# Kernel optimization log

Measured on AMD Instinct MI355X. Metric: run time of the kernel, lower is better.

The kernel has to match this reference:

```python
import jax, jax.numpy as jnp
import numpy as np

B, N, D, H = 2, 2048, 384, 8
Dh = D // H          # 48
G = Dh // 3          # 16 3-vectors per head
EPS = 1e-5


def setup_inputs() -> dict:
    key = jax.random.key(0)
    ks = jax.random.split(key, 8)
    x = jax.random.normal(ks[0], (B, N, D), dtype=jnp.float32)
    # per-node SE(3) frames: proper rotation matrices via QR of random Gaussians
    raw = jax.random.normal(ks[1], (B, N, 3, 3), dtype=jnp.float32)
    q, r = jnp.linalg.qr(raw)
    sign = jnp.sign(jnp.diagonal(r, axis1=-2, axis2=-1))
    frames = q * sign[..., None, :]
    s = 1.0 / np.sqrt(D)
    Wq = jax.random.normal(ks[2], (D, D), dtype=jnp.float32) * s
    Wk = jax.random.normal(ks[3], (D, D), dtype=jnp.float32) * s
    Wv = jax.random.normal(ks[4], (D, D), dtype=jnp.float32) * s
    Wo = jax.random.normal(ks[5], (D, D), dtype=jnp.float32) * s
    bo = jnp.zeros((D,), dtype=jnp.float32)
    gamma = jnp.ones((D,), dtype=jnp.float32)
    beta = jnp.zeros((D,), dtype=jnp.float32)
    return {"x": x, "frames": frames, "Wq": Wq, "Wk": Wk, "Wv": Wv,
            "Wo": Wo, "bo": bo, "gamma": gamma, "beta": beta}


def _rotate(frames, t):
    # t: [B,N,H,Dh] -> rotate each 3-vector chunk by the node's frame R_i
    b, n, h, dh = t.shape
    t3 = t.reshape(b, n, h, dh // 3, 3)
    r3 = jnp.einsum('bnij,bnhgj->bnhgi', frames, t3)
    return r3.reshape(b, n, h, dh)


def reference(x, frames, Wq, Wk, Wv, Wo, bo, gamma, beta):
    b, n, d = x.shape
    Q = (x @ Wq.T).reshape(b, n, H, Dh)
    K = (x @ Wk.T).reshape(b, n, H, Dh)
    V = (x @ Wv.T).reshape(b, n, H, Dh)
    # SE(3) frame-conditioned attention: rotate Q,K into each node's local frame
    Qr = _rotate(frames, Q)
    Kr = _rotate(frames, K)
    scores = jnp.einsum('bqhd,bkhd->bhqk', Qr, Kr) / np.sqrt(Dh)
    attn = jax.nn.softmax(scores, axis=-1)
    out = jnp.einsum('bhqk,bkhd->bqhd', attn, V).reshape(b, n, d)
    out = out @ Wo.T + bo          # out_proj; dropout is identity in eval
    y = x + out                     # residual
    mu = jnp.mean(y, axis=-1, keepdims=True)
    var = jnp.var(y, axis=-1, keepdims=True)
    return (y - mu) * jax.lax.rsqrt(var + EPS) * gamma + beta
```

## Files before the change

kernel.cpp:

```cpp
#include <hip/hip_runtime.h>
#include <hip/hip_bf16.h>
#include <math.h>

constexpr int B = 2, N = 2048, D = 384, H = 8, Dh = 48;
constexpr int M = B * N;
constexpr float EPS = 1e-5f;
constexpr int WSZ = 384 * 384;

typedef short bf16x8 __attribute__((ext_vector_type(8)));
typedef float f32x4 __attribute__((ext_vector_type(4)));

#if __has_builtin(__builtin_amdgcn_exp2f)
#define EXP2(x) __builtin_amdgcn_exp2f(x)
#else
#define EXP2(x) exp2f(x)
#endif

__device__ __forceinline__ ushort f2bf(float f) {
  union { float f; uint u; } v; v.f = f;
  uint r = v.u + 0x7fffu + ((v.u >> 16) & 1u);
  return (ushort)(r >> 16);
}
__device__ __forceinline__ float bf2f(ushort u) {
  union { uint u; float f; } v; v.u = ((uint)u) << 16;
  return v.f;
}
__device__ __forceinline__ uint pk_bf16(float lo, float hi) {
  union { __hip_bfloat162 h; uint u; } v;
  v.h = __float22bfloat162_rn(make_float2(lo, hi));
  return v.u;
}

__device__ __forceinline__ void gload16(const void* g, void* lds) {
  __builtin_amdgcn_global_load_lds(
      (const __attribute__((address_space(1))) unsigned int*)g,
      (__attribute__((address_space(3))) unsigned int*)lds, 16, 0, 0);
}

__global__ __launch_bounds__(256) void pack_all(
    const float* __restrict__ x, const float* __restrict__ Wq,
    const float* __restrict__ Wk, const float* __restrict__ Wv,
    const float* __restrict__ Wo, ushort* __restrict__ xbf,
    ushort* __restrict__ Wqkv, ushort* __restrict__ Wobf) {
  constexpr int XSZ = M * 384;
  int i = (blockIdx.x * 256 + threadIdx.x) * 8;
  const float* src; ushort* dst; int off;
  if (i < XSZ) { src = x; dst = xbf; off = i; }
  else {
    int j = i - XSZ;
    if (j < WSZ)          { src = Wq; dst = Wqkv;           off = j; }
    else if (j < 2 * WSZ) { src = Wk; dst = Wqkv + WSZ;     off = j - WSZ; }
    else if (j < 3 * WSZ) { src = Wv; dst = Wqkv + 2 * WSZ; off = j - 2 * WSZ; }
    else                  { src = Wo; dst = Wobf;           off = j - 3 * WSZ; }
  }
  float4 a = *(const float4*)(src + off);
  float4 b = *(const float4*)(src + off + 4);
  uint4 o;
  o.x = pk_bf16(a.x, a.y);
  o.y = pk_bf16(a.z, a.w);
  o.z = pk_bf16(b.x, b.y);
  o.w = pk_bf16(b.z, b.w);
  *(uint4*)(dst + off) = o;
}

__global__ __launch_bounds__(256) void gemm_qkv(
    const ushort* __restrict__ Abf, const ushort* __restrict__ Wbf,
    ushort* __restrict__ Qpad, ushort* __restrict__ Kpad,
    ushort* __restrict__ Vt) {
  __shared__ ushort Asm[128 * 32];
  __shared__ ushort Bsm[128 * 32];
  const int tid = threadIdx.x, w = tid >> 6, lane = tid & 63;
  const int lq = lane & 15, g = lane >> 4;
  const int brow = blockIdx.y * 128, bcol = blockIdx.x * 128;
  const int wr0 = (w >> 1) * 64, wc0 = (w & 1) * 64;
  const int srow = lane >> 2, scol = (lane & 3) * 8;
  f32x4 acc[4][4];
#pragma unroll
  for (int mi = 0; mi < 4; ++mi)
#pragma unroll
    for (int ni = 0; ni < 4; ++ni) acc[mi][ni] = f32x4{0.f, 0.f, 0.f, 0.f};

  for (int kt = 0; kt < 384; kt += 32) {
    __syncthreads();
#pragma unroll
    for (int i = 0; i < 2; ++i) {
      int seg = w * 2 + i;
      gload16(Abf + (size_t)(brow + seg * 16 + srow) * 384 + kt + scol, Asm + seg * 512);
      gload16(Wbf + (size_t)(bcol + seg * 16 + srow) * 384 + kt + scol, Bsm + seg * 512);
    }
    __syncthreads();
    bf16x8 a[4], b[4];
#pragma unroll
    for (int mi = 0; mi < 4; ++mi)
      a[mi] = *(const bf16x8*)(Asm + (wr0 + mi * 16 + lq) * 32 + g * 8);
#pragma unroll
    for (int ni = 0; ni < 4; ++ni)
      b[ni] = *(const bf16x8*)(Bsm + (wc0 + ni * 16 + lq) * 32 + g * 8);
#pragma unroll
    for (int mi = 0; mi < 4; ++mi)
#pragma unroll
      for (int ni = 0; ni < 4; ++ni)
        acc[mi][ni] = __builtin_amdgcn_mfma_f32_16x16x32_bf16(a[mi], b[ni], acc[mi][ni], 0, 0, 0);
  }

  if (bcol < 768) {
#pragma unroll
    for (int mi = 0; mi < 4; ++mi)
#pragma unroll
      for (int ni = 0; ni < 4; ++ni) {
        int colD = bcol + wc0 + ni * 16 + lq;
        ushort* dstm = (colD < 384) ? Qpad : Kpad;
        int c = (colD < 384) ? colD : colD - 384;
        int hh = c / 48, dh = c - hh * 48;
#pragma unroll
        for (int r = 0; r < 4; ++r) {
          int row = brow + wr0 + mi * 16 + g * 4 + r;
          dstm[(size_t)row * 512 + hh * 64 + dh] = f2bf(acc[mi][ni][r]);
        }
      }
  } else {
#pragma unroll
    for (int mi = 0; mi < 4; ++mi)
#pragma unroll
      for (int ni = 0; ni < 4; ++ni) {
        int vcol = bcol + wc0 + ni * 16 + lq - 768;
        int hh = vcol / 48, dh = vcol - hh * 48;
#pragma unroll
        for (int r = 0; r < 4; ++r) {
          int row = brow + wr0 + mi * 16 + g * 4 + r;
          int bb = row >> 11, nn = row & 2047;
          Vt[((size_t)(bb * H + hh) * 48 + dh) * N + nn] = f2bf(acc[mi][ni][r]);
        }
      }
  }
}

__global__ __launch_bounds__(256) void rotate_both(
    ushort* __restrict__ Q, ushort* __restrict__ K,
    const float* __restrict__ F, float qscale) {
  constexpr int TOT = M * H * 16;
  int idx = blockIdx.x * 256 + threadIdx.x;
  ushort* T = (idx < TOT) ? Q : K;
  float scale = (idx < TOT) ? qscale : 1.0f;
  int rem = (idx < TOT) ? idx : idx - TOT;
  int gq = rem & 15;
  int nh = rem >> 4;
  int h = nh & 7;
  int bn = nh >> 3;
  ushort* p = T + (size_t)bn * 512 + h * 64;
  if (gq < 8) *(uint*)(p + 48 + gq * 2) = 0u;
  ushort* s = p + gq * 3;
  const float* R = F + (size_t)bn * 9;
  float v0 = bf2f(s[0]), v1 = bf2f(s[1]), v2 = bf2f(s[2]);
  float w0 = (R[0] * v0 + R[1] * v1 + R[2] * v2) * scale;
  float w1 = (R[3] * v0 + R[4] * v1 + R[5] * v2) * scale;
  float w2 = (R[6] * v0 + R[7] * v1 + R[8] * v2) * scale;
  s[0] = f2bf(w0); s[1] = f2bf(w1); s[2] = f2bf(w2);
}

__global__ __launch_bounds__(256) void attn_mfma(
    const ushort* __restrict__ Qpad, const ushort* __restrict__ Kpad,
    const ushort* __restrict__ Vt, ushort* __restrict__ Pacc,
    float* __restrict__ Pml) {
  __shared__ ushort K_lds[2][64 * 64];
  __shared__ ushort V_lds[2][48 * 64];
  __shared__ ushort P_lds[4][16 * 64];

  const int bid = blockIdx.x;
  const int wg = (bid & 7) * 128 + (bid >> 3);
  const int qt = wg & 31;
  const int rest = wg >> 5;
  const int h = rest & 7;
  const int b = (rest >> 3) & 1;
  const int half = rest >> 4;
  const int kt0 = half * 1024;
  const int tid = threadIdx.x;
  const int w = tid >> 6;
  const int lane = tid & 63;
  const int lq = lane & 15;
  const int g = lane >> 4;
  const int l7 = lq & 7;
  const int srow8 = lane >> 3;
  const int csw = (lane & 7) ^ srow8;

  const ushort* qp = Qpad + (size_t)(b * N + qt * 64 + w * 16 + lq) * 512 + h * 64;
  bf16x8 qf0 = *(const bf16x8*)(qp + g * 8);
  bf16x8 qf1 = *(const bf16x8*)(qp + 32 + g * 8);

  const ushort* kg0 = Kpad + (size_t)(b * N) * 512 + h * 64
                    + (size_t)(kt0 + w * 8 + srow8) * 512 + csw * 8;
  const ushort* kg1 = kg0 + 32 * 512;
  const ushort* vg0 = Vt + ((size_t)(b * H + h) * 48 + w * 8 + srow8) * (size_t)N
                    + kt0 + csw * 8;
  const ushort* vg1 = vg0 + 32 * (size_t)N;

  auto stage = [&](int buf) {
    gload16(kg0, &K_lds[buf][w * 512]);
    gload16(kg1, &K_lds[buf][(w + 4) * 512]);
    gload16(vg0, &V_lds[buf][w * 512]);
    if (w < 2) gload16(vg1, &V_lds[buf][(w + 4) * 512]);
    kg0 += 64 * 512; kg1 += 64 * 512; vg0 += 64; vg1 += 64;
  };

  float m = -3.0e38f, l = 0.f;
  f32x4 oacc[3];
#pragma unroll
  for (int d = 0; d < 3; ++d) oacc[d] = f32x4{0.f, 0.f, 0.f, 0.f};

  stage(0);
  __syncthreads();
  int cur = 0;

  for (int t = 0; t < 16; ++t) {
    if (t < 15) stage(cur ^ 1);

    const ushort* Kc = K_lds[cur];
    const ushort* Vc = V_lds[cur];

    f32x4 st[4];
#pragma unroll
    for (int t4 = 0; t4 < 4; ++t4) st[t4] = f32x4{0.f, 0.f, 0.f, 0.f};
#pragma unroll
    for (int t4 = 0; t4 < 4; ++t4) {
      int row = t4 * 16 + lq;
      bf16x8 a0 = *(const bf16x8*)(Kc + row * 64 + ((g ^ l7) * 8));
      st[t4] = __builtin_amdgcn_mfma_f32_16x16x32_bf16(a0, qf0, st[t4], 0, 0, 0);
      bf16x8 a1 = *(const bf16x8*)(Kc + row * 64 + (((g ^ 4) ^ l7) * 8));
      st[t4] = __builtin_amdgcn_mfma_f32_16x16x32_bf16(a1, qf1, st[t4], 0, 0, 0);
    }

    float tmax = st[0][0];
#pragma unroll
    for (int t4 = 0; t4 < 4; ++t4)
#pragma unroll
      for (int r = 0; r < 4; ++r) tmax = fmaxf(tmax, st[t4][r]);
    tmax = fmaxf(tmax, __shfl_xor(tmax, 16));
    tmax = fmaxf(tmax, __shfl_xor(tmax, 32));

    if (__ballot(tmax > m + 8.0f)) {
      float mnew = fmaxf(m, tmax);
      float corr = EXP2(m - mnew);
      m = mnew;
      l *= corr;
#pragma unroll
      for (int r = 0; r < 4; ++r) {
        float cr = __shfl(corr, g * 4 + r);
#pragma unroll
        for (int d = 0; d < 3; ++d) oacc[d][r] *= cr;
      }
    }

    float psum = 0.f;
#pragma unroll
    for (int t4 = 0; t4 < 4; ++t4) {
      float p0 = EXP2(st[t4][0] - m);
      float p1 = EXP2(st[t4][1] - m);
      float p2 = EXP2(st[t4][2] - m);
      float p3 = EXP2(st[t4][3] - m);
      psum += (p0 + p1) + (p2 + p3);
      uint2 pk;
      pk.x = pk_bf16(p0, p1);
      pk.y = pk_bf16(p2, p3);
      *(uint2*)(P_lds[w] + lq * 64 + (((2 * t4 + (g >> 1)) ^ l7) * 8) + (g & 1) * 4) = pk;
    }
    psum += __shfl_xor(psum, 16);
    psum += __shfl_xor(psum, 32);
    l += psum;

#pragma unroll
    for (int ks = 0; ks < 2; ++ks) {
      bf16x8 pf = *(const bf16x8*)(P_lds[w] + lq * 64 + ((((ks << 2) | g) ^ l7) * 8));
#pragma unroll
      for (int d = 0; d < 3; ++d) {
        bf16x8 vf = *(const bf16x8*)(Vc + (d * 16 + lq) * 64 + ((((ks << 2) | g) ^ l7) * 8));
        oacc[d] = __builtin_amdgcn_mfma_f32_16x16x32_bf16(pf, vf, oacc[d], 0, 0, 0);
      }
    }

    __syncthreads();
    cur ^= 1;
  }

  const size_t pr0 = ((size_t)((half * B + b) * H + h)) * N + qt * 64 + w * 16;
#pragma unroll
  for (int d = 0; d < 3; ++d)
#pragma unroll
    for (int r = 0; r < 4; ++r)
      Pacc[(pr0 + g * 4 + r) * 48 + d * 16 + lq] = f2bf(oacc[d][r]);
  if (g == 0) {
    Pml[(pr0 + lq) * 2] = m;
    Pml[(pr0 + lq) * 2 + 1] = l;
  }
}

__global__ __launch_bounds__(256) void attn_merge(
    const ushort* __restrict__ Pacc, const float* __restrict__ Pml,
    ushort* __restrict__ Obf) {
  int idx = blockIdx.x * 256 + threadIdx.x;
  int h = idx & 7, bn = idx >> 3;
  int b = bn >> 11, n = bn & 2047;
  size_t r0 = ((size_t)(b * H + h)) * N + n;
  size_t r1 = ((size_t)((B + b) * H + h)) * N + n;
  float m0 = Pml[r0 * 2], l0 = Pml[r0 * 2 + 1];
  float m1 = Pml[r1 * 2], l1 = Pml[r1 * 2 + 1];
  float mm = fmaxf(m0, m1);
  float w0 = EXP2(m0 - mm), w1 = EXP2(m1 - mm);
  float inv = 1.f / (l0 * w0 + l1 * w1);
  w0 *= inv; w1 *= inv;
  const ushort* p0 = Pacc + r0 * 48;
  const ushort* p1 = Pacc + r1 * 48;
  ushort* ob = Obf + (size_t)bn * 384 + h * 48;
#pragma unroll
  for (int j = 0; j < 6; ++j) {
    uint4 a = *(const uint4*)(p0 + j * 8);
    uint4 c = *(const uint4*)(p1 + j * 8);
    uint4 o;
    o.x = pk_bf16(bf2f((ushort)a.x) * w0 + bf2f((ushort)c.x) * w1,
                  bf2f((ushort)(a.x >> 16)) * w0 + bf2f((ushort)(c.x >> 16)) * w1);
    o.y = pk_bf16(bf2f((ushort)a.y) * w0 + bf2f((ushort)c.y) * w1,
                  bf2f((ushort)(a.y >> 16)) * w0 + bf2f((ushort)(c.y >> 16)) * w1);
    o.z = pk_bf16(bf2f((ushort)a.z) * w0 + bf2f((ushort)c.z) * w1,
                  bf2f((ushort)(a.z >> 16)) * w0 + bf2f((ushort)(c.z >> 16)) * w1);
    o.w = pk_bf16(bf2f((ushort)a.w) * w0 + bf2f((ushort)c.w) * w1,
                  bf2f((ushort)(a.w >> 16)) * w0 + bf2f((ushort)(c.w >> 16)) * w1);
    *(uint4*)(ob + j * 8) = o;
  }
}

__global__ __launch_bounds__(256) void gemm_out_ln(
    const ushort* __restrict__ Abf, const ushort* __restrict__ Wbf,
    const float* __restrict__ x, const float* __restrict__ bo,
    const float* __restrict__ gamma, const float* __restrict__ beta,
    float* __restrict__ out) {
  __shared__ ushort Asm[64 * 32];
  __shared__ ushort Bsm[384 * 32];
  const int tid = threadIdx.x, w = tid >> 6, lane = tid & 63;
  const int lq = lane & 15, g = lane >> 4;
  const int brow = blockIdx.x * 64;
  const int srow = lane >> 2, scol = (lane & 3) * 8;
  f32x4 acc[24];
#pragma unroll
  for (int ni = 0; ni < 24; ++ni) acc[ni] = f32x4{0.f, 0.f, 0.f, 0.f};

  for (int kt = 0; kt < 384; kt += 32) {
    __syncthreads();
    gload16(Abf + (size_t)(brow + w * 16 + srow) * 384 + kt + scol, Asm + w * 512);
#pragma unroll
    for (int i = 0; i < 6; ++i) {
      int seg = w * 6 + i;
      gload16(Wbf + (size_t)(seg * 16 + srow) * 384 + kt + scol, Bsm + seg * 512);
    }
    __syncthreads();
    bf16x8 a = *(const bf16x8*)(Asm + (w * 16 + lq) * 32 + g * 8);
#pragma unroll
    for (int ni = 0; ni < 24; ++ni) {
      bf16x8 bfr = *(const bf16x8*)(Bsm + (ni * 16 + lq) * 32 + g * 8);
      acc[ni] = __builtin_amdgcn_mfma_f32_16x16x32_bf16(a, bfr, acc[ni], 0, 0, 0);
    }
  }

  const int row0 = brow + w * 16 + g * 4;
#pragma unroll
  for (int r = 0; r < 4; ++r) {
    const float* xr = x + (size_t)(row0 + r) * 384;
    float s = 0.f, s2 = 0.f;
#pragma unroll
    for (int ni = 0; ni < 24; ++ni) {
      int col = ni * 16 + lq;
      float y = acc[ni][r] + xr[col] + bo[col];
      acc[ni][r] = y;
      s += y; s2 += y * y;
    }
#pragma unroll
    for (int o = 1; o < 16; o <<= 1) {
      s += __shfl_xor(s, o);
      s2 += __shfl_xor(s2, o);
    }
    float mu = s * (1.f / 384.f);
    float var = s2 * (1.f / 384.f) - mu * mu;
    float rstd = rsqrtf(var + EPS);
    float* orow = out + (size_t)(row0 + r) * 384;
#pragma unroll
    for (int ni = 0; ni < 24; ++ni) {
      int col = ni * 16 + lq;
      orow[col] = (acc[ni][r] - mu) * rstd * gamma[col] + beta[col];
    }
  }
}

extern "C" void kernel_launch(void* const* d_in, const int* in_sizes, int n_in,
                              void* d_out, int out_size, void* d_ws, size_t ws_size,
                              hipStream_t stream) {
  const float* x      = (const float*)d_in[0];
  const float* frames = (const float*)d_in[1];
  const float* Wq     = (const float*)d_in[2];
  const float* Wk     = (const float*)d_in[3];
  const float* Wv     = (const float*)d_in[4];
  const float* Wo     = (const float*)d_in[5];
  const float* bo     = (const float*)d_in[6];
  const float* gamma  = (const float*)d_in[7];
  const float* beta   = (const float*)d_in[8];
  float* out = (float*)d_out;

  ushort* xbf  = (ushort*)d_ws;
  ushort* Obf  = xbf;
  ushort* Wqkv = xbf + (size_t)M * 384;
  ushort* Wobf = Wqkv + 3 * (size_t)WSZ;
  ushort* Qpad = Wobf + (size_t)WSZ;
  ushort* Kpad = Qpad + (size_t)M * 512;
  ushort* Vt   = Kpad + (size_t)M * 512;
  ushort* Pacc = Vt + (size_t)M * 384;
  float*  Pml  = (float*)(Pacc + (size_t)2 * B * H * N * 48);

  const float qscale = 0.14433756729740643f * 1.4426950408889634f;

  pack_all<<<(M * 384 + 4 * WSZ) / (8 * 256), 256, 0, stream>>>(
      x, Wq, Wk, Wv, Wo, xbf, Wqkv, Wobf);

  gemm_qkv<<<dim3(9, 32), 256, 0, stream>>>(xbf, Wqkv, Qpad, Kpad, Vt);

  rotate_both<<<2 * M * H * 16 / 256, 256, 0, stream>>>(Qpad, Kpad, frames, qscale);

  attn_mfma<<<2 * B * H * (N / 64), 256, 0, stream>>>(Qpad, Kpad, Vt, Pacc, Pml);

  attn_merge<<<M * H / 256, 256, 0, stream>>>(Pacc, Pml, Obf);

  gemm_out_ln<<<M / 64, 256, 0, stream>>>(Obf, Wobf, x, bo, gamma, beta, out);
}
```

Baseline: 86.45 us.

## Split keys across waves in attention and shrink QKV GEMM row tile

The attention kernel now has every wave hold all 64 query rows of the tile and process its own 16-key slice of each 64-key block. Per-wave partial softmax states are merged through LDS at the end, and P·V uses a 16x16x16 MFMA straight from registers, which removes the P round trip through LDS. The QKV GEMM row tile drops from 128 to 64, doubling the grid to give more blocks to the CUs. In exchange, each wave keeps more accumulator registers live and the kernel does an extra cross-wave reduction, with bf16 rounding of the partial outputs before the merge.

```diff
diff --git a/kernel.cpp b/kernel.cpp
--- a/kernel.cpp
+++ b/kernel.cpp
@@ -8,12 +8,20 @@
 constexpr int WSZ = 384 * 384;
 
 typedef short bf16x8 __attribute__((ext_vector_type(8)));
+typedef short bf16x4 __attribute__((ext_vector_type(4)));
 typedef float f32x4 __attribute__((ext_vector_type(4)));
 
 #if __has_builtin(__builtin_amdgcn_exp2f)
 #define EXP2(x) __builtin_amdgcn_exp2f(x)
 #else
 #define EXP2(x) exp2f(x)
+#endif
+
+#if __has_builtin(__builtin_amdgcn_mfma_f32_16x16x16bf16_1k)
+#define HAVE_MFMA16 1
+#define MFMA16(a, b, c) __builtin_amdgcn_mfma_f32_16x16x16bf16_1k(a, b, c, 0, 0, 0)
+#else
+#define HAVE_MFMA16 0
 #endif
 
 __device__ __forceinline__ ushort f2bf(float f) {
@@ -67,37 +75,37 @@
     const ushort* __restrict__ Abf, const ushort* __restrict__ Wbf,
     ushort* __restrict__ Qpad, ushort* __restrict__ Kpad,
     ushort* __restrict__ Vt) {
-  __shared__ ushort Asm[128 * 32];
+  __shared__ ushort Asm[64 * 32];
   __shared__ ushort Bsm[128 * 32];
   const int tid = threadIdx.x, w = tid >> 6, lane = tid & 63;
   const int lq = lane & 15, g = lane >> 4;
-  const int brow = blockIdx.y * 128, bcol = blockIdx.x * 128;
-  const int wr0 = (w >> 1) * 64, wc0 = (w & 1) * 64;
+  const int brow = blockIdx.y * 64, bcol = blockIdx.x * 128;
+  const int wr0 = (w >> 1) * 32, wc0 = (w & 1) * 64;
   const int srow = lane >> 2, scol = (lane & 3) * 8;
-  f32x4 acc[4][4];
-#pragma unroll
-  for (int mi = 0; mi < 4; ++mi)
+  f32x4 acc[2][4];
+#pragma unroll
+  for (int mi = 0; mi < 2; ++mi)
 #pragma unroll
     for (int ni = 0; ni < 4; ++ni) acc[mi][ni] = f32x4{0.f, 0.f, 0.f, 0.f};
 
   for (int kt = 0; kt < 384; kt += 32) {
     __syncthreads();
+    gload16(Abf + (size_t)(brow + w * 16 + srow) * 384 + kt + scol, Asm + w * 512);
 #pragma unroll
     for (int i = 0; i < 2; ++i) {
       int seg = w * 2 + i;
-      gload16(Abf + (size_t)(brow + seg * 16 + srow) * 384 + kt + scol, Asm + seg * 512);
       gload16(Wbf + (size_t)(bcol + seg * 16 + srow) * 384 + kt + scol, Bsm + seg * 512);
     }
     __syncthreads();
-    bf16x8 a[4], b[4];
-#pragma unroll
-    for (int mi = 0; mi < 4; ++mi)
+    bf16x8 a[2], b[4];
+#pragma unroll
+    for (int mi = 0; mi < 2; ++mi)
       a[mi] = *(const bf16x8*)(Asm + (wr0 + mi * 16 + lq) * 32 + g * 8);
 #pragma unroll
     for (int ni = 0; ni < 4; ++ni)
       b[ni] = *(const bf16x8*)(Bsm + (wc0 + ni * 16 + lq) * 32 + g * 8);
 #pragma unroll
-    for (int mi = 0; mi < 4; ++mi)
+    for (int mi = 0; mi < 2; ++mi)
 #pragma unroll
       for (int ni = 0; ni < 4; ++ni)
         acc[mi][ni] = __builtin_amdgcn_mfma_f32_16x16x32_bf16(a[mi], b[ni], acc[mi][ni], 0, 0, 0);
@@ -105,7 +113,7 @@
 
   if (bcol < 768) {
 #pragma unroll
-    for (int mi = 0; mi < 4; ++mi)
+    for (int mi = 0; mi < 2; ++mi)
 #pragma unroll
       for (int ni = 0; ni < 4; ++ni) {
         int colD = bcol + wc0 + ni * 16 + lq;
@@ -120,7 +128,7 @@
       }
   } else {
 #pragma unroll
-    for (int mi = 0; mi < 4; ++mi)
+    for (int mi = 0; mi < 2; ++mi)
 #pragma unroll
       for (int ni = 0; ni < 4; ++ni) {
         int vcol = bcol + wc0 + ni * 16 + lq - 768;
@@ -162,9 +170,14 @@
     const ushort* __restrict__ Qpad, const ushort* __restrict__ Kpad,
     const ushort* __restrict__ Vt, ushort* __restrict__ Pacc,
     float* __restrict__ Pml) {
-  __shared__ ushort K_lds[2][64 * 64];
-  __shared__ ushort V_lds[2][48 * 64];
-  __shared__ ushort P_lds[4][16 * 64];
+  __shared__ __align__(16) ushort SH[16384];
+  ushort* Kb0 = SH;
+  ushort* Kb1 = SH + 4096;
+  ushort* Vb0 = SH + 8192;
+  ushort* Vb1 = SH + 11264;
+#if !HAVE_MFMA16
+  ushort* Psc = SH + 14336;
+#endif
 
   const int bid = blockIdx.x;
   const int wg = (bid & 7) * 128 + (bid >> 3);
@@ -179,117 +192,195 @@
   const int lane = tid & 63;
   const int lq = lane & 15;
   const int g = lane >> 4;
-  const int l7 = lq & 7;
   const int srow8 = lane >> 3;
   const int csw = (lane & 7) ^ srow8;
-
-  const ushort* qp = Qpad + (size_t)(b * N + qt * 64 + w * 16 + lq) * 512 + h * 64;
-  bf16x8 qf0 = *(const bf16x8*)(qp + g * 8);
-  bf16x8 qf1 = *(const bf16x8*)(qp + 32 + g * 8);
-
-  const ushort* kg0 = Kpad + (size_t)(b * N) * 512 + h * 64
-                    + (size_t)(kt0 + w * 8 + srow8) * 512 + csw * 8;
+  const int vsw = (lane & 7) ^ ((4 * (w & 1) + (srow8 >> 1)) & 7);
+
+#if !HAVE_MFMA16
+  if (g < 2) {
+    uint4 z = make_uint4(0, 0, 0, 0);
+    *(uint4*)(Psc + w * 512 + lq * 32 + 16 + g * 8) = z;
+  }
+#endif
+
+  bf16x8 qf[4][2];
+  {
+    const ushort* qb = Qpad + (size_t)(b * N + qt * 64) * 512 + h * 64;
+#pragma unroll
+    for (int qg = 0; qg < 4; ++qg)
+#pragma unroll
+      for (int ks = 0; ks < 2; ++ks)
+        qf[qg][ks] = *(const bf16x8*)(qb + (size_t)(qg * 16 + lq) * 512 + ks * 32 + g * 8);
+  }
+
+  const ushort* kg0 = Kpad + ((size_t)(b * N) + kt0 + w * 8 + srow8) * 512 + h * 64 + csw * 8;
   const ushort* kg1 = kg0 + 32 * 512;
-  const ushort* vg0 = Vt + ((size_t)(b * H + h) * 48 + w * 8 + srow8) * (size_t)N
-                    + kt0 + csw * 8;
+  const ushort* vg0 = Vt + ((size_t)(b * H + h) * 48 + w * 8 + srow8) * (size_t)N + kt0 + vsw * 8;
   const ushort* vg1 = vg0 + 32 * (size_t)N;
 
-  auto stage = [&](int buf) {
-    gload16(kg0, &K_lds[buf][w * 512]);
-    gload16(kg1, &K_lds[buf][(w + 4) * 512]);
-    gload16(vg0, &V_lds[buf][w * 512]);
-    if (w < 2) gload16(vg1, &V_lds[buf][(w + 4) * 512]);
+  auto stage = [&](ushort* kb, ushort* vb) {
+    gload16(kg0, kb + w * 512);
+    gload16(kg1, kb + (w + 4) * 512);
+    gload16(vg0, vb + w * 512);
+    if (w < 2) gload16(vg1, vb + (w + 4) * 512);
     kg0 += 64 * 512; kg1 += 64 * 512; vg0 += 64; vg1 += 64;
   };
 
-  float m = -3.0e38f, l = 0.f;
-  f32x4 oacc[3];
-#pragma unroll
-  for (int d = 0; d < 3; ++d) oacc[d] = f32x4{0.f, 0.f, 0.f, 0.f};
-
-  stage(0);
+  float m[4], l[4];
+  f32x4 oacc[4][3];
+#pragma unroll
+  for (int qg = 0; qg < 4; ++qg) {
+    m[qg] = -3.0e38f; l[qg] = 0.f;
+#pragma unroll
+    for (int d = 0; d < 3; ++d) oacc[qg][d] = f32x4{0.f, 0.f, 0.f, 0.f};
+  }
+
+  stage(Kb0, Vb0);
   __syncthreads();
   int cur = 0;
 
   for (int t = 0; t < 16; ++t) {
-    if (t < 15) stage(cur ^ 1);
-
-    const ushort* Kc = K_lds[cur];
-    const ushort* Vc = V_lds[cur];
+    if (t < 15) stage(cur ? Kb0 : Kb1, cur ? Vb0 : Vb1);
+    const ushort* Kc = cur ? Kb1 : Kb0;
+    const ushort* Vc = cur ? Vb1 : Vb0;
+
+    bf16x8 kf0 = *(const bf16x8*)(Kc + (w * 16 + lq) * 64 + ((g ^ (lq & 7)) * 8));
+    bf16x8 kf1 = *(const bf16x8*)(Kc + (w * 16 + lq) * 64 + (((4 + g) ^ (lq & 7)) * 8));
 
     f32x4 st[4];
 #pragma unroll
-    for (int t4 = 0; t4 < 4; ++t4) st[t4] = f32x4{0.f, 0.f, 0.f, 0.f};
-#pragma unroll
-    for (int t4 = 0; t4 < 4; ++t4) {
-      int row = t4 * 16 + lq;
-      bf16x8 a0 = *(const bf16x8*)(Kc + row * 64 + ((g ^ l7) * 8));
-      st[t4] = __builtin_amdgcn_mfma_f32_16x16x32_bf16(a0, qf0, st[t4], 0, 0, 0);
-      bf16x8 a1 = *(const bf16x8*)(Kc + row * 64 + (((g ^ 4) ^ l7) * 8));
-      st[t4] = __builtin_amdgcn_mfma_f32_16x16x32_bf16(a1, qf1, st[t4], 0, 0, 0);
-    }
-
-    float tmax = st[0][0];
-#pragma unroll
-    for (int t4 = 0; t4 < 4; ++t4)
-#pragma unroll
-      for (int r = 0; r < 4; ++r) tmax = fmaxf(tmax, st[t4][r]);
-    tmax = fmaxf(tmax, __shfl_xor(tmax, 16));
-    tmax = fmaxf(tmax, __shfl_xor(tmax, 32));
-
-    if (__ballot(tmax > m + 8.0f)) {
-      float mnew = fmaxf(m, tmax);
-      float corr = EXP2(m - mnew);
-      m = mnew;
-      l *= corr;
-#pragma unroll
-      for (int r = 0; r < 4; ++r) {
-        float cr = __shfl(corr, g * 4 + r);
-#pragma unroll
-        for (int d = 0; d < 3; ++d) oacc[d][r] *= cr;
+    for (int qg = 0; qg < 4; ++qg) {
+      st[qg] = f32x4{0.f, 0.f, 0.f, 0.f};
+      st[qg] = __builtin_amdgcn_mfma_f32_16x16x32_bf16(kf0, qf[qg][0], st[qg], 0, 0, 0);
+      st[qg] = __builtin_amdgcn_mfma_f32_16x16x32_bf16(kf1, qf[qg][1], st[qg], 0, 0, 0);
+    }
+
+#if HAVE_MFMA16
+    bf16x4 vb[3];
+#pragma unroll
+    for (int d = 0; d < 3; ++d)
+      vb[d] = *(const bf16x4*)(Vc + (d * 16 + lq) * 64 + (((w * 4 + g) ^ (lq & 14)) * 4));
+#endif
+
+    float tmax[4];
+    bool need = false;
+#pragma unroll
+    for (int qg = 0; qg < 4; ++qg) {
+      float t0 = fmaxf(fmaxf(st[qg][0], st[qg][1]), fmaxf(st[qg][2], st[qg][3]));
+      t0 = fmaxf(t0, __shfl_xor(t0, 16));
+      t0 = fmaxf(t0, __shfl_xor(t0, 32));
+      tmax[qg] = t0;
+      need |= (t0 > m[qg] + 8.0f);
+    }
+    if (__ballot(need)) {
+#pragma unroll
+      for (int qg = 0; qg < 4; ++qg) {
+        float mnew = fmaxf(m[qg], tmax[qg]);
+        float corr = EXP2(m[qg] - mnew);
+        m[qg] = mnew;
+        l[qg] *= corr;
+#pragma unroll
+        for (int r = 0; r < 4; ++r) {
+          float cr = __shfl(corr, g * 4 + r);
+#pragma unroll
+          for (int d = 0; d < 3; ++d) oacc[qg][d][r] *= cr;
+        }
       }
     }
 
-    float psum = 0.f;
-#pragma unroll
-    for (int t4 = 0; t4 < 4; ++t4) {
-      float p0 = EXP2(st[t4][0] - m);
-      float p1 = EXP2(st[t4][1] - m);
-      float p2 = EXP2(st[t4][2] - m);
-      float p3 = EXP2(st[t4][3] - m);
-      psum += (p0 + p1) + (p2 + p3);
-      uint2 pk;
-      pk.x = pk_bf16(p0, p1);
-      pk.y = pk_bf16(p2, p3);
-      *(uint2*)(P_lds[w] + lq * 64 + (((2 * t4 + (g >> 1)) ^ l7) * 8) + (g & 1) * 4) = pk;
-    }
-    psum += __shfl_xor(psum, 16);
-    psum += __shfl_xor(psum, 32);
-    l += psum;
-
-#pragma unroll
-    for (int ks = 0; ks < 2; ++ks) {
-      bf16x8 pf = *(const bf16x8*)(P_lds[w] + lq * 64 + ((((ks << 2) | g) ^ l7) * 8));
+#pragma unroll
+    for (int qg = 0; qg < 4; ++qg) {
+      float p0 = EXP2(st[qg][0] - m[qg]);
+      float p1 = EXP2(st[qg][1] - m[qg]);
+      float p2 = EXP2(st[qg][2] - m[qg]);
+      float p3 = EXP2(st[qg][3] - m[qg]);
+      float ps = (p0 + p1) + (p2 + p3);
+      ps += __shfl_xor(ps, 16);
+      ps += __shfl_xor(ps, 32);
+      l[qg] += ps;
+#if HAVE_MFMA16
+      union { uint2 u; bf16x4 v; } pw;
+      pw.u.x = pk_bf16(p0, p1);
+      pw.u.y = pk_bf16(p2, p3);
+#pragma unroll
+      for (int d = 0; d < 3; ++d)
+        oacc[qg][d] = MFMA16(pw.v, vb[d], oacc[qg][d]);
+#else
+      uint2 pu; pu.x = pk_bf16(p0, p1); pu.y = pk_bf16(p2, p3);
+      *(uint2*)(Psc + w * 512 + lq * 32 + g * 4) = pu;
+      bf16x8 pf = *(const bf16x8*)(Psc + w * 512 + lq * 32 + g * 8);
 #pragma unroll
       for (int d = 0; d < 3; ++d) {
-        bf16x8 vf = *(const bf16x8*)(Vc + (d * 16 + lq) * 64 + ((((ks << 2) | g) ^ l7) * 8));
-        oacc[d] = __builtin_amdgcn_mfma_f32_16x16x32_bf16(pf, vf, oacc[d], 0, 0, 0);
+        bf16x8 vf = *(const bf16x8*)(Vc + (d * 16 + lq) * 64 +
+                                     (((w * 2 + g) ^ ((lq >> 1) & 7)) * 8));
+        oacc[qg][d] = __builtin_amdgcn_mfma_f32_16x16x32_bf16(pf, vf, oacc[qg][d], 0, 0, 0);
       }
+#endif
     }
 
     __syncthreads();
     cur ^= 1;
   }
 
+  uint2* Om = (uint2*)SH;
+  float2* Ml = (float2*)(SH + 12288);
+#pragma unroll
+  for (int qg = 0; qg < 4; ++qg)
+#pragma unroll
+    for (int d = 0; d < 3; ++d) {
+      uint2 u;
+      u.x = pk_bf16(oacc[qg][d][0], oacc[qg][d][1]);
+      u.y = pk_bf16(oacc[qg][d][2], oacc[qg][d][3]);
+      Om[((w * 4 + qg) * 3 + d) * 64 + g * 16 + lq] = u;
+    }
+  if (g == 0) {
+#pragma unroll
+    for (int qg = 0; qg < 4; ++qg)
+      Ml[(w * 4 + qg) * 16 + lq] = make_float2(m[qg], l[qg]);
+  }
+  __syncthreads();
+
+  float mp[4][4], lp[4][4];
+#pragma unroll
+  for (int wp = 0; wp < 4; ++wp)
+#pragma unroll
+    for (int r = 0; r < 4; ++r) {
+      float2 t2 = Ml[(wp * 4 + w) * 16 + g * 4 + r];
+      mp[wp][r] = t2.x; lp[wp][r] = t2.y;
+    }
+  float Mx[4], Lt[4], Wt[4][4];
+#pragma unroll
+  for (int r = 0; r < 4; ++r) {
+    Mx[r] = fmaxf(fmaxf(mp[0][r], mp[1][r]), fmaxf(mp[2][r], mp[3][r]));
+    Lt[r] = 0.f;
+#pragma unroll
+    for (int wp = 0; wp < 4; ++wp) {
+      Wt[wp][r] = EXP2(mp[wp][r] - Mx[r]);
+      Lt[r] += lp[wp][r] * Wt[wp][r];
+    }
+  }
   const size_t pr0 = ((size_t)((half * B + b) * H + h)) * N + qt * 64 + w * 16;
 #pragma unroll
-  for (int d = 0; d < 3; ++d)
+  for (int d = 0; d < 3; ++d) {
+    float od[4] = {0.f, 0.f, 0.f, 0.f};
+#pragma unroll
+    for (int wp = 0; wp < 4; ++wp) {
+      uint2 u = Om[((wp * 4 + w) * 3 + d) * 64 + g * 16 + lq];
+      od[0] += bf2f((ushort)u.x) * Wt[wp][0];
+      od[1] += bf2f((ushort)(u.x >> 16)) * Wt[wp][1];
+      od[2] += bf2f((ushort)u.y) * Wt[wp][2];
+      od[3] += bf2f((ushort)(u.y >> 16)) * Wt[wp][3];
+    }
 #pragma unroll
     for (int r = 0; r < 4; ++r)
-      Pacc[(pr0 + g * 4 + r) * 48 + d * 16 + lq] = f2bf(oacc[d][r]);
-  if (g == 0) {
-    Pml[(pr0 + lq) * 2] = m;
-    Pml[(pr0 + lq) * 2 + 1] = l;
+      Pacc[(pr0 + g * 4 + r) * 48 + d * 16 + lq] = f2bf(od[r]);
+  }
+  if (lq == 0) {
+#pragma unroll
+    for (int r = 0; r < 4; ++r) {
+      Pml[(pr0 + g * 4 + r) * 2] = Mx[r];
+      Pml[(pr0 + g * 4 + r) * 2 + 1] = Lt[r];
+    }
   }
 }
 
@@ -417,7 +508,7 @@
   pack_all<<<(M * 384 + 4 * WSZ) / (8 * 256), 256, 0, stream>>>(
       x, Wq, Wk, Wv, Wo, xbf, Wqkv, Wobf);
 
-  gemm_qkv<<<dim3(9, 32), 256, 0, stream>>>(xbf, Wqkv, Qpad, Kpad, Vt);
+  gemm_qkv<<<dim3(9, 64), 256, 0, stream>>>(xbf, Wqkv, Qpad, Kpad, Vt);
 
   rotate_both<<<2 * M * H * 16 / 256, 256, 0, stream>>>(Qpad, Kpad, frames, qscale);
 
```

Result: slower. 101.1 us (+16.9%).
